# Optimization experiments

Hardware: AMD Instinct MI355X
Metric: run time of the kernel (lower is better)

## Reference

```python
import jax, jax.numpy as jnp
import numpy as np

F = 256          # number of features (input_size)
H1, H2, H3 = 128, 64, 32
OUT = 1          # output_size


def setup_inputs() -> dict:
    key = jax.random.key(0)
    ks = jax.random.split(key, 10)
    B = 8192
    # Kaiming-uniform-ish small init; exact init doesn't matter for a math reference.
    def w(k, shape, fan_in):
        lim = 1.0 / np.sqrt(fan_in)
        return jax.random.uniform(k, shape, jnp.float32, -lim, lim)
    return {
        "x": jax.random.normal(ks[0], (B, F), dtype=jnp.float32),
        "W1": w(ks[1], (F, H1), 1),          # Linear(1 -> H1) per feature
        "b1": w(ks[2], (F, H1), 1),
        "W2": w(ks[3], (F, H1, H2), H1),
        "b2": w(ks[4], (F, H2), H1),
        "W3": w(ks[5], (F, H2, H3), H2),
        "b3": w(ks[6], (F, H3), H2),
        "W4": w(ks[7], (F, H3, OUT), H3),
        "b4": w(ks[8], (F, OUT), H3),
        "bias": jnp.zeros((OUT,), dtype=jnp.float32),
    }


def reference(x, W1, b1, W2, b2, W3, b3, W4, b4, bias):
    # Fused form of the per-feature FeatureNN loop (eval mode: dropout = identity).
    # Layer 1: scalar input per feature -> H1
    h = jax.nn.relu(x[:, :, None] * W1[None, :, :] + b1[None, :, :])   # [B,F,H1]
    h = jax.nn.relu(jnp.einsum('bfh,fhk->bfk', h, W2) + b2[None])      # [B,F,H2]
    h = jax.nn.relu(jnp.einsum('bfh,fhk->bfk', h, W3) + b3[None])      # [B,F,H3]
    f_out = jnp.einsum('bfh,fhk->bfk', h, W4) + b4[None]               # [B,F,OUT]
    # torch.cat(dim=1).sum(dim=1, keepdim=True): sum over features and output cols
    out = jnp.sum(f_out, axis=(1, 2), keepdims=False)[:, None] + bias[None, :]
    return out  # [B, OUT] with OUT==1
```

## Files before the change

### kernel.cpp

```cpp
#include <hip/hip_runtime.h>
#include <math.h>


#define NF   256
#define NH1  128
#define NH2  64
#define NH3  32
#define NB   8192

#define NRANK 129
#define ROW4  17
#define ROWH  136

typedef float    f32x16 __attribute__((ext_vector_type(16)));
typedef unsigned u32x4  __attribute__((ext_vector_type(4)));
typedef _Float16 h16x2  __attribute__((ext_vector_type(2)));
typedef _Float16 h16x8  __attribute__((ext_vector_type(8)));

__device__ __forceinline__ unsigned pkh2(unsigned sw, unsigned sb, h16x2 xh) {
    h16x2 r = __builtin_elementwise_fma(xh, __builtin_bit_cast(h16x2, sw),
                                            __builtin_bit_cast(h16x2, sb));
    h16x2 hz = {(_Float16)0.f, (_Float16)0.f};
    return __builtin_bit_cast(unsigned, __builtin_elementwise_max(r, hz));
}

__global__ __launch_bounds__(1024) void transpose_x(
    const float* __restrict__ x, const float* __restrict__ bias,
    float* __restrict__ out, float* __restrict__ xt)
{
    __shared__ float xtile[64][65];
    const int t = (int)threadIdx.x;
    const int T = blockIdx.x;
    const int bt = T >> 2, ft = T & 3;

    if (T < 8) out[T * 1024 + t] = bias[0];

    #pragma unroll
    for (int it = 0; it < 4; ++it) {
        int idx = t + it * 1024;
        int rr = idx >> 6, cc = idx & 63;
        xtile[rr][cc] = x[(size_t)(bt * 64 + rr) * NF + ft * 64 + cc];
    }
    __syncthreads();
    #pragma unroll
    for (int it = 0; it < 4; ++it) {
        int idx = t + it * 1024;
        int cc = idx >> 6, rr = idx & 63;
        xt[(size_t)(ft * 64 + cc) * NB + bt * 64 + rr] = xtile[rr][cc];
    }
}

__global__ __launch_bounds__(1024) void nam_fused(
    const float* __restrict__ W1, const float* __restrict__ b1,
    const float* __restrict__ W2, const float* __restrict__ b2,
    const float* __restrict__ W3, const float* __restrict__ b3,
    const float* __restrict__ W4, const float* __restrict__ b4,
    const float* __restrict__ xt,
    float* __restrict__ out)
{
    __shared__ u32x4 SP4[NRANK * ROW4];
    __shared__ float rkey[NH1];
    __shared__ float skey[NH1];
    __shared__ int   sidx[NH1];
    __shared__ float w1s[NH1], b1s[NH1];
    __shared__ float Pbw[16][NH2], Pbb[16][NH2], Pdw[16][NH2], Pdb[16][NH2];

    const int f = blockIdx.x;
    const int t = (int)threadIdx.x;
    _Float16* SPh = (_Float16*)SP4;

    const float* __restrict__ gw2 = W2 + (size_t)f * NH1 * NH2;
    if (t < NH1) {
        float w  = W1[f * NH1 + t];
        float bb = b1[f * NH1 + t];
        w1s[t] = w; b1s[t] = bb;
        rkey[t] = (w != 0.0f) ? (-bb / w) : INFINITY;
    }
    __syncthreads();

    if (t < NH1) {
        const float my = rkey[t];
        int rk = 0;
        #pragma unroll 16
        for (int i = 0; i < NH1; ++i) {
            float ki = rkey[i];
            rk += (ki < my || (ki == my && i < t)) ? 1 : 0;
        }
        skey[rk] = my; sidx[rk] = t;
    }
    __syncthreads();

    {
        const int k = t & 63, c = t >> 6;
        float bw = 0.0f, bbp = 0.0f, dw = 0.0f, db = 0.0f;
        #pragma unroll
        for (int i = 0; i < 8; ++i) {
            int j = c * 8 + i;
            float w = w1s[j], bv = b1s[j], w2v = gw2[j * NH2 + k];
            if (w < 0.0f) { bw = fmaf(w, w2v, bw); bbp = fmaf(bv, w2v, bbp); }
            else if (w == 0.0f && bv > 0.0f) { bbp = fmaf(bv, w2v, bbp); }
            int jj = sidx[c * 8 + i];
            float ww = w1s[jj], bv2 = b1s[jj], w2x = gw2[jj * NH2 + k];
            float s = (ww > 0.0f) ? 1.0f : ((ww < 0.0f) ? -1.0f : 0.0f);
            dw = fmaf(s * ww,  w2x, dw);
            db = fmaf(s * bv2, w2x, db);
        }
        Pbw[c][k] = bw; Pbb[c][k] = bbp; Pdw[c][k] = dw; Pdb[c][k] = db;
    }
    __syncthreads();
    {
        const int k = t & 63, c = t >> 6;
        float accw = 0.0f;
        float accb = b2[f * NH2 + k];
        #pragma unroll
        for (int c2 = 0; c2 < 16; ++c2) { accw += Pbw[c2][k]; accb += Pbb[c2][k]; }
        for (int c2 = 0; c2 < c; ++c2) { accw += Pdw[c2][k]; accb += Pdb[c2][k]; }
        if (c == 0) {
            SPh[k]      = (_Float16)accw;
            SPh[64 + k] = (_Float16)accb;
        }
        #pragma unroll
        for (int i = 0; i < 8; ++i) {
            int r = c * 8 + i;
            int j = sidx[r];
            float w = w1s[j], bv = b1s[j], w2v = gw2[j * NH2 + k];
            float s = (w > 0.0f) ? 1.0f : ((w < 0.0f) ? -1.0f : 0.0f);
            accw = fmaf(s * w,  w2v, accw);
            accb = fmaf(s * bv, w2v, accb);
            SPh[(r + 1) * ROWH + k]      = (_Float16)accw;
            SPh[(r + 1) * ROWH + 64 + k] = (_Float16)accb;
        }
    }
    __syncthreads();

    const int lane = t & 63, wv = t >> 6;
    const int n = lane & 31, q2 = lane >> 5;

    const float* __restrict__ w3g = W3 + f * NH2 * NH3;
    h16x8 A0, A1, A2, A3;
    #pragma unroll
    for (int j = 0; j < 8; ++j) {
        int kk = q2 * 8 + j;
        A0[j] = (_Float16)w3g[kk * NH3 + n];
        A1[j] = (_Float16)w3g[(kk + 16) * NH3 + n];
        A2[j] = (_Float16)w3g[(kk + 32) * NH3 + n];
        A3[j] = (_Float16)w3g[(kk + 48) * NH3 + n];
    }
    f32x16 bacc;
    float w4r[16];
    #pragma unroll
    for (int reg = 0; reg < 16; ++reg) {
        int row = (reg & 3) + 8 * (reg >> 2) + 4 * q2;
        bacc[reg] = b3[f * NH3 + row];
        w4r[reg]  = W4[f * NH3 + row];
    }
    const float b4f = b4[f];
    const float* __restrict__ xrow = xt + (size_t)f * NB;
    const float t63 = skey[63], t31 = skey[31], t95 = skey[95];
    const float t15 = skey[15], t47 = skey[47], t79 = skey[79], t111 = skey[111];

    auto rankof = [&](float q) -> int {
        int rr = (t63 < q) ? 64 : 0;
        {
            float l1 = (rr & 64) ? t95 : t31;
            if (l1 < q) rr += 32;
            float m0 = (rr & 64) ? t79  : t15;
            float m1 = (rr & 64) ? t111 : t47;
            float l2 = (rr & 32) ? m1 : m0;
            if (l2 < q) rr += 16;
        }
        #pragma unroll
        for (int s = 8; s > 0; s >>= 1)
            if (skey[rr + s - 1] < q) rr += s;
        return rr;
    };

    const int boff = wv * 32 + n;
    float xv = xrow[((0 + f) & 15) * 512 + boff];
    int r = rankof(xv);

    #pragma unroll 1
    for (int round = 0; round < 16; ++round) {
        const int base = (((round + f) & 15) * 16 + wv) * 32;
        const float xnext = xrow[(((round + 1 + f) & 15) * 16 + wv) * 32 + n];

        const int ro = r * ROW4;
        u32x4 SW0 = SP4[ro + q2],      SW1 = SP4[ro + 2 + q2];
        u32x4 SW2 = SP4[ro + 4 + q2],  SW3 = SP4[ro + 6 + q2];
        u32x4 SB0 = SP4[ro + 8 + q2],  SB1 = SP4[ro + 10 + q2];
        u32x4 SB2 = SP4[ro + 12 + q2], SB3 = SP4[ro + 14 + q2];

        const h16x2 xh = {(_Float16)xv, (_Float16)xv};
        u32x4 d0, d1, d2, d3;
        d0.x = pkh2(SW0.x, SB0.x, xh); d0.y = pkh2(SW0.y, SB0.y, xh);
        d0.z = pkh2(SW0.z, SB0.z, xh); d0.w = pkh2(SW0.w, SB0.w, xh);
        d1.x = pkh2(SW1.x, SB1.x, xh); d1.y = pkh2(SW1.y, SB1.y, xh);
        d1.z = pkh2(SW1.z, SB1.z, xh); d1.w = pkh2(SW1.w, SB1.w, xh);
        d2.x = pkh2(SW2.x, SB2.x, xh); d2.y = pkh2(SW2.y, SB2.y, xh);
        d2.z = pkh2(SW2.z, SB2.z, xh); d2.w = pkh2(SW2.w, SB2.w, xh);
        d3.x = pkh2(SW3.x, SB3.x, xh); d3.y = pkh2(SW3.y, SB3.y, xh);
        d3.z = pkh2(SW3.z, SB3.z, xh); d3.w = pkh2(SW3.w, SB3.w, xh);
        h16x8 B0 = __builtin_bit_cast(h16x8, d0);
        h16x8 B1 = __builtin_bit_cast(h16x8, d1);
        h16x8 B2 = __builtin_bit_cast(h16x8, d2);
        h16x8 B3 = __builtin_bit_cast(h16x8, d3);

        f32x16 acc = __builtin_amdgcn_mfma_f32_32x32x16_f16(A0, B0, bacc, 0, 0, 0);
        acc = __builtin_amdgcn_mfma_f32_32x32x16_f16(A1, B1, acc, 0, 0, 0);
        acc = __builtin_amdgcn_mfma_f32_32x32x16_f16(A2, B2, acc, 0, 0, 0);
        acc = __builtin_amdgcn_mfma_f32_32x32x16_f16(A3, B3, acc, 0, 0, 0);

        const int rnext = rankof(xnext);

        float p = 0.0f;
        #pragma unroll
        for (int reg = 0; reg < 16; ++reg)
            p = fmaf(fmaxf(acc[reg], 0.0f), w4r[reg], p);
        p += __shfl_xor(p, 32);
        if (lane < 32) atomicAdd(&out[base + lane], p + b4f);

        xv = xnext; r = rnext;
    }
}

extern "C" void kernel_launch(void* const* d_in, const int* in_sizes, int n_in,
                              void* d_out, int out_size, void* d_ws, size_t ws_size,
                              hipStream_t stream) {
    const float* x    = (const float*)d_in[0];
    const float* W1   = (const float*)d_in[1];
    const float* b1   = (const float*)d_in[2];
    const float* W2   = (const float*)d_in[3];
    const float* b2   = (const float*)d_in[4];
    const float* W3   = (const float*)d_in[5];
    const float* b3   = (const float*)d_in[6];
    const float* W4   = (const float*)d_in[7];
    const float* b4   = (const float*)d_in[8];
    const float* bias = (const float*)d_in[9];
    float* out   = (float*)d_out;
    float* xtw   = (float*)d_ws;

    transpose_x<<<512, 1024, 0, stream>>>(x, bias, out, xtw);
    nam_fused<<<NF, 1024, 0, stream>>>(W1, b1, W2, b2, W3, b3, W4, b4, xtw, out);
}
```

Measured before the change: 111.7 us.

## Drop x transpose kernel and read x strided directly; repack LDS table rows

Removes the separate transpose pre-pass, so the main kernel reads x[b*NF+f] directly with a stride of NF floats per lane, and a tiny kernel only initializes out with the bias. The LDS table of packed weight/bias halves changes from 17 u32x4 per row to 66 dwords per row, read with 64-bit loads to change the bank-conflict pattern. This saves one kernel launch and a round trip of x through memory, but the x reads are now uncoalesced, although each 32-byte sector is shared by neighbouring feature blocks through cache.

```diff
diff --git a/kernel.cpp b/kernel.cpp
--- a/kernel.cpp
+++ b/kernel.cpp
@@ -9,8 +9,8 @@
 #define NB   8192
 
 #define NRANK 129
-#define ROW4  17
-#define ROWH  136
+#define ROWDW 66
+#define ROWH  132
 
 typedef float    f32x16 __attribute__((ext_vector_type(16)));
 typedef unsigned u32x4  __attribute__((ext_vector_type(4)));
@@ -24,30 +24,10 @@
     return __builtin_bit_cast(unsigned, __builtin_elementwise_max(r, hz));
 }
 
-__global__ __launch_bounds__(1024) void transpose_x(
-    const float* __restrict__ x, const float* __restrict__ bias,
-    float* __restrict__ out, float* __restrict__ xt)
+__global__ __launch_bounds__(1024) void init_out(
+    const float* __restrict__ bias, float* __restrict__ out)
 {
-    __shared__ float xtile[64][65];
-    const int t = (int)threadIdx.x;
-    const int T = blockIdx.x;
-    const int bt = T >> 2, ft = T & 3;
-
-    if (T < 8) out[T * 1024 + t] = bias[0];
-
-    #pragma unroll
-    for (int it = 0; it < 4; ++it) {
-        int idx = t + it * 1024;
-        int rr = idx >> 6, cc = idx & 63;
-        xtile[rr][cc] = x[(size_t)(bt * 64 + rr) * NF + ft * 64 + cc];
-    }
-    __syncthreads();
-    #pragma unroll
-    for (int it = 0; it < 4; ++it) {
-        int idx = t + it * 1024;
-        int cc = idx >> 6, rr = idx & 63;
-        xt[(size_t)(ft * 64 + cc) * NB + bt * 64 + rr] = xtile[rr][cc];
-    }
+    out[blockIdx.x * 1024 + threadIdx.x] = bias[0];
 }
 
 __global__ __launch_bounds__(1024) void nam_fused(
@@ -55,10 +35,10 @@
     const float* __restrict__ W2, const float* __restrict__ b2,
     const float* __restrict__ W3, const float* __restrict__ b3,
     const float* __restrict__ W4, const float* __restrict__ b4,
-    const float* __restrict__ xt,
+    const float* __restrict__ x,
     float* __restrict__ out)
 {
-    __shared__ u32x4 SP4[NRANK * ROW4];
+    __shared__ unsigned SPD[NRANK * ROWDW];
     __shared__ float rkey[NH1];
     __shared__ float skey[NH1];
     __shared__ int   sidx[NH1];
@@ -67,7 +47,7 @@
 
     const int f = blockIdx.x;
     const int t = (int)threadIdx.x;
-    _Float16* SPh = (_Float16*)SP4;
+    _Float16* SPh = (_Float16*)SPD;
 
     const float* __restrict__ gw2 = W2 + (size_t)f * NH1 * NH2;
     if (t < NH1) {
@@ -155,7 +135,6 @@
         w4r[reg]  = W4[f * NH3 + row];
     }
     const float b4f = b4[f];
-    const float* __restrict__ xrow = xt + (size_t)f * NB;
     const float t63 = skey[63], t31 = skey[31], t95 = skey[95];
     const float t15 = skey[15], t47 = skey[47], t79 = skey[79], t111 = skey[111];
 
@@ -175,31 +154,37 @@
         return rr;
     };
 
-    const int boff = wv * 32 + n;
-    float xv = xrow[((0 + f) & 15) * 512 + boff];
+    auto bat = [&](int round) -> int {
+        return (((round + f) & 15) * 16 + wv) * 32 + n;
+    };
+    float xv = x[(size_t)bat(0) * NF + f];
     int r = rankof(xv);
 
     #pragma unroll 1
     for (int round = 0; round < 16; ++round) {
         const int base = (((round + f) & 15) * 16 + wv) * 32;
-        const float xnext = xrow[(((round + 1 + f) & 15) * 16 + wv) * 32 + n];
-
-        const int ro = r * ROW4;
-        u32x4 SW0 = SP4[ro + q2],      SW1 = SP4[ro + 2 + q2];
-        u32x4 SW2 = SP4[ro + 4 + q2],  SW3 = SP4[ro + 6 + q2];
-        u32x4 SB0 = SP4[ro + 8 + q2],  SB1 = SP4[ro + 10 + q2];
-        u32x4 SB2 = SP4[ro + 12 + q2], SB3 = SP4[ro + 14 + q2];
+        const float xnext = x[(size_t)bat((round + 1) & 15) * NF + f];
+
+        const int rb = r * ROWDW + 4 * q2;
+        uint2 SW0a = *(const uint2*)&SPD[rb +  0], SW0b = *(const uint2*)&SPD[rb +  2];
+        uint2 SW1a = *(const uint2*)&SPD[rb +  8], SW1b = *(const uint2*)&SPD[rb + 10];
+        uint2 SW2a = *(const uint2*)&SPD[rb + 16], SW2b = *(const uint2*)&SPD[rb + 18];
+        uint2 SW3a = *(const uint2*)&SPD[rb + 24], SW3b = *(const uint2*)&SPD[rb + 26];
+        uint2 SB0a = *(const uint2*)&SPD[rb + 32], SB0b = *(const uint2*)&SPD[rb + 34];
+        uint2 SB1a = *(const uint2*)&SPD[rb + 40], SB1b = *(const uint2*)&SPD[rb + 42];
+        uint2 SB2a = *(const uint2*)&SPD[rb + 48], SB2b = *(const uint2*)&SPD[rb + 50];
+        uint2 SB3a = *(const uint2*)&SPD[rb + 56], SB3b = *(const uint2*)&SPD[rb + 58];
 
         const h16x2 xh = {(_Float16)xv, (_Float16)xv};
         u32x4 d0, d1, d2, d3;
-        d0.x = pkh2(SW0.x, SB0.x, xh); d0.y = pkh2(SW0.y, SB0.y, xh);
-        d0.z = pkh2(SW0.z, SB0.z, xh); d0.w = pkh2(SW0.w, SB0.w, xh);
-        d1.x = pkh2(SW1.x, SB1.x, xh); d1.y = pkh2(SW1.y, SB1.y, xh);
-        d1.z = pkh2(SW1.z, SB1.z, xh); d1.w = pkh2(SW1.w, SB1.w, xh);
-        d2.x = pkh2(SW2.x, SB2.x, xh); d2.y = pkh2(SW2.y, SB2.y, xh);
-        d2.z = pkh2(SW2.z, SB2.z, xh); d2.w = pkh2(SW2.w, SB2.w, xh);
-        d3.x = pkh2(SW3.x, SB3.x, xh); d3.y = pkh2(SW3.y, SB3.y, xh);
-        d3.z = pkh2(SW3.z, SB3.z, xh); d3.w = pkh2(SW3.w, SB3.w, xh);
+        d0.x = pkh2(SW0a.x, SB0a.x, xh); d0.y = pkh2(SW0a.y, SB0a.y, xh);
+        d0.z = pkh2(SW0b.x, SB0b.x, xh); d0.w = pkh2(SW0b.y, SB0b.y, xh);
+        d1.x = pkh2(SW1a.x, SB1a.x, xh); d1.y = pkh2(SW1a.y, SB1a.y, xh);
+        d1.z = pkh2(SW1b.x, SB1b.x, xh); d1.w = pkh2(SW1b.y, SB1b.y, xh);
+        d2.x = pkh2(SW2a.x, SB2a.x, xh); d2.y = pkh2(SW2a.y, SB2a.y, xh);
+        d2.z = pkh2(SW2b.x, SB2b.x, xh); d2.w = pkh2(SW2b.y, SB2b.y, xh);
+        d3.x = pkh2(SW3a.x, SB3a.x, xh); d3.y = pkh2(SW3a.y, SB3a.y, xh);
+        d3.z = pkh2(SW3b.x, SB3b.x, xh); d3.w = pkh2(SW3b.y, SB3b.y, xh);
         h16x8 B0 = __builtin_bit_cast(h16x8, d0);
         h16x8 B1 = __builtin_bit_cast(h16x8, d1);
         h16x8 B2 = __builtin_bit_cast(h16x8, d2);
@@ -237,8 +222,8 @@
     const float* b4   = (const float*)d_in[8];
     const float* bias = (const float*)d_in[9];
     float* out   = (float*)d_out;
-    float* xtw   = (float*)d_ws;
-
-    transpose_x<<<512, 1024, 0, stream>>>(x, bias, out, xtw);
-    nam_fused<<<NF, 1024, 0, stream>>>(W1, b1, W2, b2, W3, b3, W4, b4, xtw, out);
-}
+    (void)d_ws; (void)ws_size;
+
+    init_out<<<NB / 1024, 1024, 0, stream>>>(bias, out);
+    nam_fused<<<NF, 1024, 0, stream>>>(W1, b1, W2, b2, W3, b3, W4, b4, x, out);
+}
```

Result: slower. 116.6 us (+4.4%).
